# Optimization experiments

Hardware: AMD Instinct MI355X
Metric: run time of the kernel (lower is better)

Reference implementation:

```python
import jax, jax.numpy as jnp
import numpy as np

HID = 64        # HIDDEN_DIM
SLOTS = 6       # MEMORY_SLOTS
V = 64          # VOCAB_SIZE
NH = 2          # attention heads
THRESH = 0.5    # STAGE1_THRESH
EPS = 1e-5      # LayerNorm eps (torch default)


def setup_inputs() -> dict:
    key = jax.random.key(0)
    ks = jax.random.split(key, 16)
    B, L = 64, 1024
    def n(k, shape, s=0.05):
        return jax.random.normal(k, shape, jnp.float32) * s
    return {
        'seq':    jax.random.randint(ks[0], (B, L), 0, V),
        'query':  jax.random.randint(ks[1], (B,), 0, V),
        'target': jax.random.randint(ks[2], (B,), 0, V),
        # TinyEncoder params
        'embed':   n(ks[3], (V, HID)),
        'wqkv':    n(ks[4], (3 * HID, HID)), 'bqkv': jnp.zeros(3 * HID, jnp.float32),
        'wo_attn': n(ks[5], (HID, HID)),     'bo_attn': jnp.zeros(HID, jnp.float32),
        'w_ff1':   n(ks[6], (2 * HID, HID)), 'b_ff1': jnp.zeros(2 * HID, jnp.float32),
        'w_ff2':   n(ks[7], (HID, 2 * HID)), 'b_ff2': jnp.zeros(HID, jnp.float32),
        'g1': jnp.ones(HID, jnp.float32), 'be1': jnp.zeros(HID, jnp.float32),
        'g2': jnp.ones(HID, jnp.float32), 'be2': jnp.zeros(HID, jnp.float32),
        # gates
        'w_s1': n(ks[8], (1, HID)), 'b_s1': jnp.zeros(1, jnp.float32),
        'w_s2': n(ks[9], (1, HID)), 'b_s2': jnp.zeros(1, jnp.float32),
        # MemoryReader
        'w_qr': n(ks[10], (HID, HID)), 'b_qr': jnp.zeros(HID, jnp.float32),
        'w_or': n(ks[11], (V, HID)),   'b_or': jnp.zeros(V, jnp.float32),
        # query embedding
        'q_embed': n(ks[12], (V, HID)),
    }


def _layernorm(x, g, b):
    m = x.mean(-1, keepdims=True)
    v = ((x - m) ** 2).mean(-1, keepdims=True)
    return (x - m) * jax.lax.rsqrt(v + EPS) * g + b


def _mha(h, wqkv, bqkv, wo, bo):
    B, L, H = h.shape
    d = H // NH
    qkv = h @ wqkv.T + bqkv                      # [B,L,3H]
    q, k, v = jnp.split(qkv, 3, axis=-1)
    q = q.reshape(B, L, NH, d)
    k = k.reshape(B, L, NH, d)
    v = v.reshape(B, L, NH, d)
    scores = jnp.einsum('bqhd,bkhd->bhqk', q, k) / jnp.sqrt(jnp.float32(d))
    w = jax.nn.softmax(scores, axis=-1)          # [B,NH,L,L]
    o = jnp.einsum('bhqk,bkhd->bqhd', w, v).reshape(B, L, H)
    return o @ wo.T + bo


def reference(seq, query, target, embed, wqkv, bqkv, wo_attn, bo_attn,
              w_ff1, b_ff1, w_ff2, b_ff2, g1, be1, g2, be2,
              w_s1, b_s1, w_s2, b_s2, w_qr, b_qr, w_or, b_or, q_embed):
    # --- TinyEncoder ---
    h = embed[seq]                                           # [B,L,H]
    a = _mha(h, wqkv, bqkv, wo_attn, bo_attn)
    h = _layernorm(h + a, g1, be1)
    ff = jax.nn.relu(h @ w_ff1.T + b_ff1) @ w_ff2.T + b_ff2
    hidden = _layernorm(h + ff, g2, be2)                     # [B,L,H]

    # --- two-stage selection (vectorized; dead s1-branch elided) ---
    s1 = jax.nn.sigmoid(jnp.squeeze(hidden @ w_s1.T + b_s1, -1))   # [B,L]
    keep = (s1 > THRESH).astype(hidden.dtype)
    s2 = jax.nn.sigmoid(jnp.squeeze(hidden @ w_s2.T + b_s2, -1))
    s2f = s2 * keep
    _, topk = jax.lax.top_k(s2f, SLOTS)                            # [B,SLOTS]

    # --- gather memory slots ---
    mem = jnp.take_along_axis(hidden, topk[:, :, None], axis=1)    # [B,SLOTS,H]

    # --- MemoryReader ---
    q_h = q_embed[query]                                           # [B,H]
    q = q_h @ w_qr.T + b_qr                                        # [B,H]
    scores = (q[:, None, :] * mem).sum(-1) / jnp.sqrt(jnp.float32(HID))  # [B,SLOTS]
    w = jax.nn.softmax(scores, axis=-1)
    ctx = (w[:, :, None] * mem).sum(1)                             # [B,H]
    logits = ctx @ w_or.T + b_or                                   # [B,V]

    # --- cross entropy (mean) ---
    logp = jax.nn.log_softmax(logits, axis=-1)
    loss = -jnp.take_along_axis(logp, target[:, None], axis=1).mean()
    return loss
```

## Files before the change

### kernel.cpp

```cpp
#include <hip/hip_runtime.h>

#define DEV __device__ __forceinline__

DEV int   f2i(float v){ return __builtin_bit_cast(int, v); }
DEV float i2f(int v){ return __builtin_bit_cast(float, v); }
DEV float blane(float v, int l){ return i2f(__builtin_amdgcn_readlane(f2i(v), l)); }

template<int C> DEV float dpp_add(float v){
  return v + i2f(__builtin_amdgcn_update_dpp(0, f2i(v), C, 0xF, 0xF, true));
}
template<int C> DEV float dpp_max(float v){
  return fmaxf(v, i2f(__builtin_amdgcn_update_dpp(0, f2i(v), C, 0xF, 0xF, true)));
}
DEV float wred_sum(float v){
  v = dpp_add<0xB1>(v); v = dpp_add<0x4E>(v); v = dpp_add<0x141>(v); v = dpp_add<0x140>(v);
  v += i2f(__builtin_amdgcn_ds_swizzle(f2i(v), 0x401F));
  return blane(v, 0) + blane(v, 32);
}
DEV float wred_max(float v){
  v = dpp_max<0xB1>(v); v = dpp_max<0x4E>(v); v = dpp_max<0x141>(v); v = dpp_max<0x140>(v);
  v = fmaxf(v, i2f(__builtin_amdgcn_ds_swizzle(f2i(v), 0x401F)));
  return fmaxf(blane(v, 0), blane(v, 32));
}

DEV float wsum(float v){
  #pragma unroll
  for (int o = 32; o; o >>= 1) v += __shfl_xor(v, o, 64);
  return v;
}
DEV float wmax(float v){
  #pragma unroll
  for (int o = 32; o; o >>= 1) v = fmaxf(v, __shfl_xor(v, o, 64));
  return v;
}

__global__ __launch_bounds__(1024) void k_prep(
    const int* __restrict__ seq, const float* __restrict__ embed,
    const float* __restrict__ wqkv, const float* __restrict__ bqkv,
    float* __restrict__ qkv_tab, float* __restrict__ cnt_f,
    float* __restrict__ out){
  const int b = blockIdx.x, tid = threadIdx.x;
  if (b == 0 && tid == 0) out[0] = 0.f;
  __shared__ float emb[64];
  __shared__ int hh[64];
  if (tid < 64){ emb[tid] = embed[b*64 + tid]; hh[tid] = 0; }
  __syncthreads();
  atomicAdd(&hh[seq[b*1024 + tid]], 1);
  if (tid < 192){
    const float4* w4 = (const float4*)(wqkv + tid*64);
    float a0 = bqkv[tid], a1 = 0.f, a2 = 0.f, a3 = 0.f;
    #pragma unroll
    for (int k = 0; k < 16; k += 4){
      float4 wa = w4[k],   wb = w4[k+1], wc = w4[k+2], wd = w4[k+3];
      a0 += wa.x*emb[4*k]    + wa.y*emb[4*k+1]  + wa.z*emb[4*k+2]  + wa.w*emb[4*k+3];
      a1 += wb.x*emb[4*k+4]  + wb.y*emb[4*k+5]  + wb.z*emb[4*k+6]  + wb.w*emb[4*k+7];
      a2 += wc.x*emb[4*k+8]  + wc.y*emb[4*k+9]  + wc.z*emb[4*k+10] + wc.w*emb[4*k+11];
      a3 += wd.x*emb[4*k+12] + wd.y*emb[4*k+13] + wd.z*emb[4*k+14] + wd.w*emb[4*k+15];
    }
    qkv_tab[b*192 + tid] = (a0+a1)+(a2+a3);
  }
  __syncthreads();
  if (tid < 64) cnt_f[b*64 + tid] = (float)hh[tid];
}

__global__ __launch_bounds__(256, 2) void k_enc(
    const float* __restrict__ qkv_tab, const float* __restrict__ cnt_f,
    const float* __restrict__ embed,
    const float* __restrict__ wo_attn, const float* __restrict__ bo_attn,
    const float* __restrict__ w_ff1, const float* __restrict__ b_ff1,
    const float* __restrict__ w_ff2, const float* __restrict__ b_ff2,
    const float* __restrict__ g1, const float* __restrict__ be1,
    const float* __restrict__ g2, const float* __restrict__ be2,
    const float* __restrict__ w_s1, const float* __restrict__ b_s1,
    const float* __restrict__ w_s2, const float* __restrict__ b_s2,
    float* __restrict__ hidden_tab, float* __restrict__ s2f_tab){
  const int b = blockIdx.x >> 2, quarter = blockIdx.x & 3;
  const int tid = threadIdx.x, w = tid >> 6, lane = tid & 63;

  __shared__ float4 k4 [64*16];
  __shared__ float4 v4t[64*16];
  __shared__ float4 wo4[64*16];
  __shared__ float4 f14[128*16];
  __shared__ float4 f24[64*32];
  __shared__ float4 pb4[4][64][2];
  __shared__ float  cnt_lds[64];

  const float4* qkv4 = (const float4*)qkv_tab;
  const float4* wo_4 = (const float4*)wo_attn;
  const float4* f1_4 = (const float4*)w_ff1;
  const float4* f2_4 = (const float4*)w_ff2;
  float* v4f = (float*)v4t;

  #pragma unroll
  for (int ii = 0; ii < 4; ++ii){
    int i = tid + ii*256;
    int r = i >> 4, c4 = i & 15, s = c4 ^ (r & 15);
    k4 [r*16 + s] = qkv4[r*48 + 16 + c4];
    wo4[r*16 + s] = wo_4[i];
    float4 vv = qkv4[r*48 + 32 + c4];
    int d0 = 4*c4;
    v4f[(d0  )*64 + 4*((r>>2) ^ ((d0  )&15)) + (r&3)] = vv.x;
    v4f[(d0+1)*64 + 4*((r>>2) ^ ((d0+1)&15)) + (r&3)] = vv.y;
    v4f[(d0+2)*64 + 4*((r>>2) ^ ((d0+2)&15)) + (r&3)] = vv.z;
    v4f[(d0+3)*64 + 4*((r>>2) ^ ((d0+3)&15)) + (r&3)] = vv.w;
  }
  #pragma unroll
  for (int ii = 0; ii < 8; ++ii){
    int i = tid + ii*256;
    int r1 = i >> 4, c41 = i & 15;
    f14[r1*16 + (c41 ^ (r1 & 15))] = f1_4[i];
    int r2 = i >> 5, c42 = i & 31;
    f24[r2*32 + (c42 ^ (r2 & 15))] = f2_4[i];
  }
  if (tid < 64) cnt_lds[tid] = cnt_f[b*64 + tid];
  __syncthreads();

  const int   t0 = quarter*16 + w*4;
  const int   sw = lane & 15;
  const int   h2 = lane >> 5;
  const float cme  = cnt_lds[lane];
  const bool  pres = cme > 0.f;
  const float sc = 0.17677669529663687f;
  const float g1v=g1[lane], be1v=be1[lane], g2v=g2[lane], be2v=be2[lane];
  const float bov=bo_attn[lane], bf2v=b_ff2[lane];
  const float bf1a=b_ff1[lane], bf1b=b_ff1[64+lane];
  const float ws1v=w_s1[lane], ws2v=w_s2[lane];
  const float bs1=b_s1[0], bs2=b_s2[0];

  float q0 = qkv_tab[(t0+0)*192 + lane];
  float q1 = qkv_tab[(t0+1)*192 + lane];
  float q2 = qkv_tab[(t0+2)*192 + lane];
  float q3 = qkv_tab[(t0+3)*192 + lane];
  float sA[4] = {0.f,0.f,0.f,0.f}, sB[4] = {0.f,0.f,0.f,0.f};
  #pragma unroll
  for (int c4 = 0; c4 < 16; ++c4){
    float4 kk = k4[lane*16 + (c4 ^ sw)];
    #pragma unroll
    for (int j = 0; j < 4; ++j){
      const int d = 4*c4 + j;
      float ke = (j==0)?kk.x:(j==1)?kk.y:(j==2)?kk.z:kk.w;
      float b0 = blane(q0,d), b1 = blane(q1,d), b2 = blane(q2,d), b3 = blane(q3,d);
      if (d < 32){ sA[0]+=b0*ke; sA[1]+=b1*ke; sA[2]+=b2*ke; sA[3]+=b3*ke; }
      else       { sB[0]+=b0*ke; sB[1]+=b1*ke; sB[2]+=b2*ke; sB[3]+=b3*ke; }
    }
  }
  float p0[4], p1[4], d0v[4], d1v[4];
  #pragma unroll
  for (int t = 0; t < 4; ++t){
    float s0 = sA[t]*sc, s1 = sB[t]*sc;
    float m0 = wred_max(pres ? s0 : -1e30f);
    float m1 = wred_max(pres ? s1 : -1e30f);
    p0[t] = pres ? cme*__expf(s0 - m0) : 0.f;
    p1[t] = pres ? cme*__expf(s1 - m1) : 0.f;
    d0v[t] = wred_sum(p0[t]);
    d1v[t] = wred_sum(p1[t]);
  }
  pb4[w][lane][0] = make_float4(p0[0],p0[1],p0[2],p0[3]);
  pb4[w][lane][1] = make_float4(p1[0],p1[1],p1[2],p1[3]);
  __builtin_amdgcn_wave_barrier();
  float o[4] = {0.f,0.f,0.f,0.f};
  #pragma unroll
  for (int c4 = 0; c4 < 16; ++c4){
    float4 vv = v4t[lane*16 + (c4 ^ sw)];
    #pragma unroll
    for (int j = 0; j < 4; ++j){
      const int tp = 4*c4 + j;
      float ve = (j==0)?vv.x:(j==1)?vv.y:(j==2)?vv.z:vv.w;
      float4 pp = pb4[w][tp][h2];
      o[0] += pp.x*ve; o[1] += pp.y*ve; o[2] += pp.z*ve; o[3] += pp.w*ve;
    }
  }
  #pragma unroll
  for (int t = 0; t < 4; ++t) o[t] /= (lane < 32 ? d0v[t] : d1v[t]);
  float aT[4] = {bov,bov,bov,bov};
  #pragma unroll
  for (int c4 = 0; c4 < 16; ++c4){
    float4 ww = wo4[lane*16 + (c4 ^ sw)];
    #pragma unroll
    for (int j = 0; j < 4; ++j){
      const int k = 4*c4 + j;
      float we = (j==0)?ww.x:(j==1)?ww.y:(j==2)?ww.z:ww.w;
      aT[0] += we*blane(o[0],k); aT[1] += we*blane(o[1],k);
      aT[2] += we*blane(o[2],k); aT[3] += we*blane(o[3],k);
    }
  }
  float xn[4];
  #pragma unroll
  for (int t = 0; t < 4; ++t){
    float x = embed[(t0+t)*64 + lane] + aT[t];
    float mu = wred_sum(x) * 0.015625f;
    float xm = x - mu;
    float var = wred_sum(xm*xm) * 0.015625f;
    xn[t] = xm * rsqrtf(var + 1e-5f) * g1v + be1v;
  }
  float y0[4] = {bf1a,bf1a,bf1a,bf1a}, y1[4] = {bf1b,bf1b,bf1b,bf1b};
  #pragma unroll
  for (int c4 = 0; c4 < 16; ++c4){
    float4 wA = f14[lane*16 + (c4 ^ sw)];
    float4 wB = f14[(lane+64)*16 + (c4 ^ sw)];
    #pragma unroll
    for (int j = 0; j < 4; ++j){
      const int k = 4*c4 + j;
      float wa = (j==0)?wA.x:(j==1)?wA.y:(j==2)?wA.z:wA.w;
      float wb = (j==0)?wB.x:(j==1)?wB.y:(j==2)?wB.z:wB.w;
      float x0 = blane(xn[0],k), x1 = blane(xn[1],k), x2 = blane(xn[2],k), x3 = blane(xn[3],k);
      y0[0]+=wa*x0; y0[1]+=wa*x1; y0[2]+=wa*x2; y0[3]+=wa*x3;
      y1[0]+=wb*x0; y1[1]+=wb*x1; y1[2]+=wb*x2; y1[3]+=wb*x3;
    }
  }
  #pragma unroll
  for (int t = 0; t < 4; ++t){ y0[t] = fmaxf(y0[t],0.f); y1[t] = fmaxf(y1[t],0.f); }
  float z[4] = {bf2v,bf2v,bf2v,bf2v};
  #pragma unroll
  for (int c4 = 0; c4 < 32; ++c4){
    float4 ww = f24[lane*32 + (c4 ^ sw)];
    #pragma unroll
    for (int j = 0; j < 4; ++j){
      const int jj = 4*c4 + j;
      float we = (j==0)?ww.x:(j==1)?ww.y:(j==2)?ww.z:ww.w;
      if (jj < 64){
        z[0]+=we*blane(y0[0],jj); z[1]+=we*blane(y0[1],jj);
        z[2]+=we*blane(y0[2],jj); z[3]+=we*blane(y0[3],jj);
      } else {
        z[0]+=we*blane(y1[0],jj-64); z[1]+=we*blane(y1[1],jj-64);
        z[2]+=we*blane(y1[2],jj-64); z[3]+=we*blane(y1[3],jj-64);
      }
    }
  }
  #pragma unroll
  for (int t = 0; t < 4; ++t){
    float r = xn[t] + z[t];
    float mu2 = wred_sum(r) * 0.015625f;
    float rm = r - mu2;
    float var2 = wred_sum(rm*rm) * 0.015625f;
    float hid = rm * rsqrtf(var2 + 1e-5f) * g2v + be2v;
    float t1 = wred_sum(hid * ws1v) + bs1;
    float t2 = wred_sum(hid * ws2v) + bs2;
    float sg1 = 1.f / (1.f + __expf(-t1));
    float sg2 = 1.f / (1.f + __expf(-t2));
    float s2f = (sg1 > 0.5f) ? sg2 : 0.f;
    hidden_tab[(b*64 + t0 + t)*64 + lane] = hid;
    if (lane == 0) s2f_tab[b*64 + t0 + t] = s2f;
  }
}

__global__ __launch_bounds__(64) void k_sel(
    const int* __restrict__ seq, const int* __restrict__ query,
    const int* __restrict__ target,
    const float* __restrict__ hidden_tab, const float* __restrict__ s2f_tab,
    const float* __restrict__ w_qr, const float* __restrict__ b_qr,
    const float* __restrict__ w_or, const float* __restrict__ b_or,
    const float* __restrict__ q_embed, float* __restrict__ out){
  const int b = blockIdx.x, lane = threadIdx.x;
  __shared__ float s2_lds[64];
  __shared__ float wq_lds[64*65];
  __shared__ float wor_lds[64*65];
  s2_lds[lane] = s2f_tab[b*64 + lane];
  #pragma unroll 8
  for (int j = 0; j < 64; ++j){
    wq_lds[j*65 + lane]  = w_qr[j*64 + lane];
    wor_lds[j*65 + lane] = w_or[j*64 + lane];
  }
  __builtin_amdgcn_wave_barrier();

  float vals[16];
  #pragma unroll
  for (int j = 0; j < 16; ++j){
    int tk = seq[b*1024 + j*64 + lane];
    vals[j] = s2_lds[tk];
  }
  int sel[6];
  #pragma unroll
  for (int r = 0; r < 6; ++r){
    float bv = -1.f; int bi = 1 << 30;
    #pragma unroll
    for (int j = 0; j < 16; ++j){
      float v = vals[j]; int i = (j << 6) | lane;
      if (v > bv || (v == bv && i < bi)){ bv = v; bi = i; }
    }
    #pragma unroll
    for (int o = 32; o; o >>= 1){
      float ov = __shfl_xor(bv, o, 64);
      int   oi = __shfl_xor(bi, o, 64);
      if (ov > bv || (ov == bv && oi < bi)){ bv = ov; bi = oi; }
    }
    sel[r] = bi;
    int jw = bi >> 6, lw = bi & 63;
    if (lane == lw){
      #pragma unroll
      for (int j = 0; j < 16; ++j) if (j == jw) vals[j] = -1.f;
    }
  }

  float mem[6];
  #pragma unroll
  for (int s = 0; s < 6; ++s){
    int tk = seq[b*1024 + sel[s]];
    mem[s] = hidden_tab[(b*64 + tk)*64 + lane];
  }
  float qe = q_embed[query[b]*64 + lane];
  float qv0 = b_qr[lane], qv1 = 0.f, qv2 = 0.f, qv3 = 0.f;
  #pragma unroll
  for (int k = 0; k < 64; k += 4){
    qv0 += wq_lds[lane*65 + k]     * __shfl(qe, k, 64);
    qv1 += wq_lds[lane*65 + k + 1] * __shfl(qe, k+1, 64);
    qv2 += wq_lds[lane*65 + k + 2] * __shfl(qe, k+2, 64);
    qv3 += wq_lds[lane*65 + k + 3] * __shfl(qe, k+3, 64);
  }
  float qv = (qv0 + qv1) + (qv2 + qv3);
  float scv[6];
  #pragma unroll
  for (int s = 0; s < 6; ++s) scv[s] = wsum(qv * mem[s]) * 0.125f;
  float mx = scv[0];
  #pragma unroll
  for (int s = 1; s < 6; ++s) mx = fmaxf(mx, scv[s]);
  float e[6], se = 0.f;
  #pragma unroll
  for (int s = 0; s < 6; ++s){ e[s] = __expf(scv[s] - mx); se += e[s]; }
  float ctx = 0.f;
  #pragma unroll
  for (int s = 0; s < 6; ++s) ctx += (e[s] / se) * mem[s];
  float l0 = b_or[lane], l1 = 0.f, l2 = 0.f, l3 = 0.f;
  #pragma unroll
  for (int k = 0; k < 64; k += 4){
    l0 += wor_lds[lane*65 + k]     * __shfl(ctx, k, 64);
    l1 += wor_lds[lane*65 + k + 1] * __shfl(ctx, k+1, 64);
    l2 += wor_lds[lane*65 + k + 2] * __shfl(ctx, k+2, 64);
    l3 += wor_lds[lane*65 + k + 3] * __shfl(ctx, k+3, 64);
  }
  float lg = (l0 + l1) + (l2 + l3);
  float lm = wmax(lg);
  float ss = wsum(__expf(lg - lm));
  float lt = __shfl(lg, target[b], 64);
  if (lane == 0) atomicAdd(out, -(lt - lm - __logf(ss)) * 0.015625f);
}

extern "C" void kernel_launch(void* const* d_in, const int* in_sizes, int n_in,
                              void* d_out, int out_size, void* d_ws, size_t ws_size,
                              hipStream_t stream){
  const int*   seq     = (const int*)  d_in[0];
  const int*   query   = (const int*)  d_in[1];
  const int*   target  = (const int*)  d_in[2];
  const float* embed   = (const float*)d_in[3];
  const float* wqkv    = (const float*)d_in[4];
  const float* bqkv    = (const float*)d_in[5];
  const float* wo_attn = (const float*)d_in[6];
  const float* bo_attn = (const float*)d_in[7];
  const float* w_ff1   = (const float*)d_in[8];
  const float* b_ff1   = (const float*)d_in[9];
  const float* w_ff2   = (const float*)d_in[10];
  const float* b_ff2   = (const float*)d_in[11];
  const float* g1      = (const float*)d_in[12];
  const float* be1     = (const float*)d_in[13];
  const float* g2      = (const float*)d_in[14];
  const float* be2     = (const float*)d_in[15];
  const float* w_s1    = (const float*)d_in[16];
  const float* b_s1    = (const float*)d_in[17];
  const float* w_s2    = (const float*)d_in[18];
  const float* b_s2    = (const float*)d_in[19];
  const float* w_qr    = (const float*)d_in[20];
  const float* b_qr    = (const float*)d_in[21];
  const float* w_or    = (const float*)d_in[22];
  const float* b_or    = (const float*)d_in[23];
  const float* q_embed = (const float*)d_in[24];

  float* ws = (float*)d_ws;
  float* qkv_tab    = ws;
  float* cnt_f      = ws + 12288;
  float* hidden_tab = ws + 16384;
  float* s2f_tab    = ws + 278528;

  float* out = (float*)d_out;

  k_prep<<<64, 1024, 0, stream>>>(seq, embed, wqkv, bqkv, qkv_tab, cnt_f, out);
  k_enc<<<256, 256, 0, stream>>>(qkv_tab, cnt_f, embed, wo_attn, bo_attn,
                                 w_ff1, b_ff1, w_ff2, b_ff2, g1, be1, g2, be2,
                                 w_s1, b_s1, w_s2, b_s2, hidden_tab, s2f_tab);
  k_sel<<<64, 64, 0, stream>>>(seq, query, target, hidden_tab, s2f_tab,
                               w_qr, b_qr, w_or, b_or, q_embed, out);
}
```

Measured before the change: 135.2 us.

## Double encoder waves per block and widen selection kernel weight staging

The encoder kernel now launches 512 threads (8 waves), and each wave handles 2 token rows instead of 4. The attention-probability broadcast now uses cross-lane readlane instead of an LDS staging buffer, which removes the pb4 shared array. The selection kernel uses 256 threads to stage its weight matrices into LDS in parallel, then keeps only one wave for the serial top-k and reader work. The aim is more parallelism per block and lower per-wave latency, at the cost of more readlane broadcasts per output and more weight-load duplication per token.

```diff
diff --git a/kernel.cpp b/kernel.cpp
--- a/kernel.cpp
+++ b/kernel.cpp
@@ -63,7 +63,7 @@
   if (tid < 64) cnt_f[b*64 + tid] = (float)hh[tid];
 }
 
-__global__ __launch_bounds__(256, 2) void k_enc(
+__global__ __launch_bounds__(512, 2) void k_enc(
     const float* __restrict__ qkv_tab, const float* __restrict__ cnt_f,
     const float* __restrict__ embed,
     const float* __restrict__ wo_attn, const float* __restrict__ bo_attn,
@@ -82,7 +82,6 @@
   __shared__ float4 wo4[64*16];
   __shared__ float4 f14[128*16];
   __shared__ float4 f24[64*32];
-  __shared__ float4 pb4[4][64][2];
   __shared__ float  cnt_lds[64];
 
   const float4* qkv4 = (const float4*)qkv_tab;
@@ -92,8 +91,8 @@
   float* v4f = (float*)v4t;
 
   #pragma unroll
-  for (int ii = 0; ii < 4; ++ii){
-    int i = tid + ii*256;
+  for (int ii = 0; ii < 2; ++ii){
+    int i = tid + ii*512;
     int r = i >> 4, c4 = i & 15, s = c4 ^ (r & 15);
     k4 [r*16 + s] = qkv4[r*48 + 16 + c4];
     wo4[r*16 + s] = wo_4[i];
@@ -105,8 +104,8 @@
     v4f[(d0+3)*64 + 4*((r>>2) ^ ((d0+3)&15)) + (r&3)] = vv.w;
   }
   #pragma unroll
-  for (int ii = 0; ii < 8; ++ii){
-    int i = tid + ii*256;
+  for (int ii = 0; ii < 4; ++ii){
+    int i = tid + ii*512;
     int r1 = i >> 4, c41 = i & 15;
     f14[r1*16 + (c41 ^ (r1 & 15))] = f1_4[i];
     int r2 = i >> 5, c42 = i & 31;
@@ -115,9 +114,8 @@
   if (tid < 64) cnt_lds[tid] = cnt_f[b*64 + tid];
   __syncthreads();
 
-  const int   t0 = quarter*16 + w*4;
+  const int   t0 = quarter*16 + w*2;
   const int   sw = lane & 15;
-  const int   h2 = lane >> 5;
   const float cme  = cnt_lds[lane];
   const bool  pres = cme > 0.f;
   const float sc = 0.17677669529663687f;
@@ -129,9 +127,7 @@
 
   float q0 = qkv_tab[(t0+0)*192 + lane];
   float q1 = qkv_tab[(t0+1)*192 + lane];
-  float q2 = qkv_tab[(t0+2)*192 + lane];
-  float q3 = qkv_tab[(t0+3)*192 + lane];
-  float sA[4] = {0.f,0.f,0.f,0.f}, sB[4] = {0.f,0.f,0.f,0.f};
+  float sA[2] = {0.f,0.f}, sB[2] = {0.f,0.f};
   #pragma unroll
   for (int c4 = 0; c4 < 16; ++c4){
     float4 kk = k4[lane*16 + (c4 ^ sw)];
@@ -139,14 +135,14 @@
     for (int j = 0; j < 4; ++j){
       const int d = 4*c4 + j;
       float ke = (j==0)?kk.x:(j==1)?kk.y:(j==2)?kk.z:kk.w;
-      float b0 = blane(q0,d), b1 = blane(q1,d), b2 = blane(q2,d), b3 = blane(q3,d);
-      if (d < 32){ sA[0]+=b0*ke; sA[1]+=b1*ke; sA[2]+=b2*ke; sA[3]+=b3*ke; }
-      else       { sB[0]+=b0*ke; sB[1]+=b1*ke; sB[2]+=b2*ke; sB[3]+=b3*ke; }
-    }
-  }
-  float p0[4], p1[4], d0v[4], d1v[4];
-  #pragma unroll
-  for (int t = 0; t < 4; ++t){
+      float b0 = blane(q0,d), b1 = blane(q1,d);
+      if (d < 32){ sA[0]+=b0*ke; sA[1]+=b1*ke; }
+      else       { sB[0]+=b0*ke; sB[1]+=b1*ke; }
+    }
+  }
+  float p0[2], p1[2], d0v[2], d1v[2];
+  #pragma unroll
+  for (int t = 0; t < 2; ++t){
     float s0 = sA[t]*sc, s1 = sB[t]*sc;
     float m0 = wred_max(pres ? s0 : -1e30f);
     float m1 = wred_max(pres ? s1 : -1e30f);
@@ -155,10 +151,7 @@
     d0v[t] = wred_sum(p0[t]);
     d1v[t] = wred_sum(p1[t]);
   }
-  pb4[w][lane][0] = make_float4(p0[0],p0[1],p0[2],p0[3]);
-  pb4[w][lane][1] = make_float4(p1[0],p1[1],p1[2],p1[3]);
-  __builtin_amdgcn_wave_barrier();
-  float o[4] = {0.f,0.f,0.f,0.f};
+  float o[2] = {0.f,0.f};
   #pragma unroll
   for (int c4 = 0; c4 < 16; ++c4){
     float4 vv = v4t[lane*16 + (c4 ^ sw)];
@@ -166,13 +159,15 @@
     for (int j = 0; j < 4; ++j){
       const int tp = 4*c4 + j;
       float ve = (j==0)?vv.x:(j==1)?vv.y:(j==2)?vv.z:vv.w;
-      float4 pp = pb4[w][tp][h2];
-      o[0] += pp.x*ve; o[1] += pp.y*ve; o[2] += pp.z*ve; o[3] += pp.w*ve;
-    }
-  }
-  #pragma unroll
-  for (int t = 0; t < 4; ++t) o[t] /= (lane < 32 ? d0v[t] : d1v[t]);
-  float aT[4] = {bov,bov,bov,bov};
+      float a0 = blane(p0[0],tp), a1 = blane(p1[0],tp);
+      float b0 = blane(p0[1],tp), b1 = blane(p1[1],tp);
+      o[0] += (lane < 32 ? a0 : a1) * ve;
+      o[1] += (lane < 32 ? b0 : b1) * ve;
+    }
+  }
+  #pragma unroll
+  for (int t = 0; t < 2; ++t) o[t] /= (lane < 32 ? d0v[t] : d1v[t]);
+  float aT[2] = {bov,bov};
   #pragma unroll
   for (int c4 = 0; c4 < 16; ++c4){
     float4 ww = wo4[lane*16 + (c4 ^ sw)];
@@ -181,19 +176,18 @@
       const int k = 4*c4 + j;
       float we = (j==0)?ww.x:(j==1)?ww.y:(j==2)?ww.z:ww.w;
       aT[0] += we*blane(o[0],k); aT[1] += we*blane(o[1],k);
-      aT[2] += we*blane(o[2],k); aT[3] += we*blane(o[3],k);
-    }
-  }
-  float xn[4];
-  #pragma unroll
-  for (int t = 0; t < 4; ++t){
+    }
+  }
+  float xn[2];
+  #pragma unroll
+  for (int t = 0; t < 2; ++t){
     float x = embed[(t0+t)*64 + lane] + aT[t];
     float mu = wred_sum(x) * 0.015625f;
     float xm = x - mu;
     float var = wred_sum(xm*xm) * 0.015625f;
     xn[t] = xm * rsqrtf(var + 1e-5f) * g1v + be1v;
   }
-  float y0[4] = {bf1a,bf1a,bf1a,bf1a}, y1[4] = {bf1b,bf1b,bf1b,bf1b};
+  float y0[2] = {bf1a,bf1a}, y1[2] = {bf1b,bf1b};
   #pragma unroll
   for (int c4 = 0; c4 < 16; ++c4){
     float4 wA = f14[lane*16 + (c4 ^ sw)];
@@ -203,14 +197,14 @@
       const int k = 4*c4 + j;
       float wa = (j==0)?wA.x:(j==1)?wA.y:(j==2)?wA.z:wA.w;
       float wb = (j==0)?wB.x:(j==1)?wB.y:(j==2)?wB.z:wB.w;
-      float x0 = blane(xn[0],k), x1 = blane(xn[1],k), x2 = blane(xn[2],k), x3 = blane(xn[3],k);
-      y0[0]+=wa*x0; y0[1]+=wa*x1; y0[2]+=wa*x2; y0[3]+=wa*x3;
-      y1[0]+=wb*x0; y1[1]+=wb*x1; y1[2]+=wb*x2; y1[3]+=wb*x3;
-    }
-  }
-  #pragma unroll
-  for (int t = 0; t < 4; ++t){ y0[t] = fmaxf(y0[t],0.f); y1[t] = fmaxf(y1[t],0.f); }
-  float z[4] = {bf2v,bf2v,bf2v,bf2v};
+      float x0 = blane(xn[0],k), x1 = blane(xn[1],k);
+      y0[0]+=wa*x0; y0[1]+=wa*x1;
+      y1[0]+=wb*x0; y1[1]+=wb*x1;
+    }
+  }
+  #pragma unroll
+  for (int t = 0; t < 2; ++t){ y0[t] = fmaxf(y0[t],0.f); y1[t] = fmaxf(y1[t],0.f); }
+  float z[2] = {bf2v,bf2v};
   #pragma unroll
   for (int c4 = 0; c4 < 32; ++c4){
     float4 ww = f24[lane*32 + (c4 ^ sw)];
@@ -220,15 +214,13 @@
       float we = (j==0)?ww.x:(j==1)?ww.y:(j==2)?ww.z:ww.w;
       if (jj < 64){
         z[0]+=we*blane(y0[0],jj); z[1]+=we*blane(y0[1],jj);
-        z[2]+=we*blane(y0[2],jj); z[3]+=we*blane(y0[3],jj);
       } else {
         z[0]+=we*blane(y1[0],jj-64); z[1]+=we*blane(y1[1],jj-64);
-        z[2]+=we*blane(y1[2],jj-64); z[3]+=we*blane(y1[3],jj-64);
       }
     }
   }
   #pragma unroll
-  for (int t = 0; t < 4; ++t){
+  for (int t = 0; t < 2; ++t){
     float r = xn[t] + z[t];
     float mu2 = wred_sum(r) * 0.015625f;
     float rm = r - mu2;
@@ -244,24 +236,26 @@
   }
 }
 
-__global__ __launch_bounds__(64) void k_sel(
+__global__ __launch_bounds__(256) void k_sel(
     const int* __restrict__ seq, const int* __restrict__ query,
     const int* __restrict__ target,
     const float* __restrict__ hidden_tab, const float* __restrict__ s2f_tab,
     const float* __restrict__ w_qr, const float* __restrict__ b_qr,
     const float* __restrict__ w_or, const float* __restrict__ b_or,
     const float* __restrict__ q_embed, float* __restrict__ out){
-  const int b = blockIdx.x, lane = threadIdx.x;
+  const int b = blockIdx.x, tid = threadIdx.x, lane = tid & 63, jr = tid >> 6;
   __shared__ float s2_lds[64];
   __shared__ float wq_lds[64*65];
   __shared__ float wor_lds[64*65];
-  s2_lds[lane] = s2f_tab[b*64 + lane];
-  #pragma unroll 8
-  for (int j = 0; j < 64; ++j){
+  if (tid < 64) s2_lds[tid] = s2f_tab[b*64 + tid];
+  #pragma unroll
+  for (int j0 = 0; j0 < 16; ++j0){
+    int j = j0*4 + jr;
     wq_lds[j*65 + lane]  = w_qr[j*64 + lane];
     wor_lds[j*65 + lane] = w_or[j*64 + lane];
   }
-  __builtin_amdgcn_wave_barrier();
+  __syncthreads();
+  if (tid >= 64) return;
 
   float vals[16];
   #pragma unroll
@@ -373,9 +367,9 @@
   float* out = (float*)d_out;
 
   k_prep<<<64, 1024, 0, stream>>>(seq, embed, wqkv, bqkv, qkv_tab, cnt_f, out);
-  k_enc<<<256, 256, 0, stream>>>(qkv_tab, cnt_f, embed, wo_attn, bo_attn,
+  k_enc<<<256, 512, 0, stream>>>(qkv_tab, cnt_f, embed, wo_attn, bo_attn,
                                  w_ff1, b_ff1, w_ff2, b_ff2, g1, be1, g2, be2,
                                  w_s1, b_s1, w_s2, b_s2, hidden_tab, s2f_tab);
-  k_sel<<<64, 64, 0, stream>>>(seq, query, target, hidden_tab, s2f_tab,
-                               w_qr, b_qr, w_or, b_or, q_embed, out);
-}
+  k_sel<<<64, 256, 0, stream>>>(seq, query, target, hidden_tab, s2f_tab,
+                                w_qr, b_qr, w_or, b_or, q_embed, out);
+}
```

New measurement: 132.3 us. -2.1%, faster.
